# Kernel tuning notes

Measured on AMD Instinct MI355X. Metric: run time of the kernel, lower is better.

## Reference

```python
import jax, jax.numpy as jnp
import numpy as np

B, C, H, W = 16, 256, 32, 32
K = 3          # kernel size
KK = K * K     # matrix_batch = 9 kernel positions
N = 256        # out_channels = n (power of 2, nstack = 1)


def setup_inputs() -> dict:
    key = jax.random.key(0)
    k1, k2, k3, k4 = jax.random.split(key, 4)
    s = 1.0 / np.sqrt(2.0)  # repo's 'regular' param init scale
    return {
        "x": jax.random.normal(k1, (B, C, H, W), jnp.float32),
        "twiddle1": jax.random.normal(k2, (KK, N - 1, 2, 2), jnp.float32) * s,
        "twiddle2": jax.random.normal(k3, (KK, N - 1, 2, 2), jnp.float32) * s,
        "bias": jax.random.normal(k4, (KK, N), jnp.float32) * 0.01,
    }


def _butterfly_tied(twiddle, x, increasing):
    """Tied-weight butterfly multiply.
    twiddle: (s, n-1, 2, 2); x: (b, s, n). At stride st, twiddle[:, st-1:2*st-1]
    (length st) is shared across the n/(2*st) blocks (matches butterfly_mult_torch).
    """
    b, s, n = x.shape
    m = n.bit_length() - 1  # log2(n)
    strides = [1 << i for i in range(m)]
    if not increasing:
        strides = strides[::-1]
    for st in strides:
        t = twiddle[:, st - 1:2 * st - 1]            # (s, st, 2, 2)
        xr = x.reshape(b, s, n // (2 * st), 2, st)   # (b, s, g, 2, st)
        # out[b,s,g,i,l] = sum_k t[s,l,i,k] * xr[b,s,g,k,l]
        x = jnp.einsum('slik,bsgkl->bsgil', t, xr).reshape(b, s, n)
    return x


def reference(x, twiddle1, twiddle2, bias):
    b, c, h, w = x.shape
    # im2col / F.unfold with kernel 3, pad 1, stride 1 -> (b, c, 9, h*w),
    # kernel positions in row-major order (matches torch unfold layout).
    xp = jnp.pad(x, ((0, 0), (0, 0), (1, 1), (1, 1)))
    patches = jnp.stack(
        [xp[:, :, i:i + h, j:j + w] for i in range(K) for j in range(K)], axis=2
    )  # (b, c, 9, h, w)
    inp = patches.reshape(b, c, KK, h * w).transpose(0, 3, 2, 1)
    inp = inp.reshape(b * h * w, KK, c)  # (batch*h*w, 9, c)
    # BB^T: B^T (decreasing stride) then B (increasing stride), bias on last.
    y = _butterfly_tied(twiddle1, inp, increasing=False)
    y = _butterfly_tied(twiddle2, y, increasing=True) + bias  # bias: (9, N)
    out = y.mean(axis=1)  # average over the 9 kernel positions -> (b*h*w, N)
    return out.reshape(b, h * w, N).transpose(0, 2, 1).reshape(b, N, h, w)
```

## Files before the change

kernel.cpp:

```cpp
#include <hip/hip_runtime.h>
#include <hip/hip_bf16.h>

typedef __attribute__((ext_vector_type(8))) short short8;
typedef __attribute__((ext_vector_type(4))) float float4v;

#define XT_ELEMS (16*34*34*256)
#define WG_ELEMS (9*4*2*8*128*8)
#define XT_BYTES (XT_ELEMS*2)
#define WG_BYTES (WG_ELEMS*2)

__global__ __launch_bounds__(256) void k_transpose(const float* __restrict__ x,
                                                   __hip_bfloat16* __restrict__ xT) {
  __shared__ float tile[256 * 33];
  int blk = blockIdx.x;
  int h = blk & 31, b = blk >> 5;
  int tid = threadIdx.x;
  {
    int w4 = (tid & 7) * 4, c0 = tid >> 3;
#pragma unroll
    for (int j = 0; j < 8; ++j) {
      int ci = c0 + 32 * j;
      float4 v = *(const float4*)&x[((b * 256 + ci) * 32 + h) * 32 + w4];
      *(float4*)&tile[ci * 33 + w4] = v;
    }
  }
  __syncthreads();
  {
    int c2 = (tid & 127) * 2, wbase = (tid >> 7) * 16;
#pragma unroll
    for (int i = 0; i < 16; ++i) {
      int w = wbase + i;
      __hip_bfloat162 pk;
      pk.x = __float2bfloat16(tile[c2 * 33 + w]);
      pk.y = __float2bfloat16(tile[(c2 + 1) * 33 + w]);
      *(__hip_bfloat162*)&xT[((b * 34 + h + 1) * 34 + (w + 1)) * 256 + c2] = pk;
    }
  }
  if (h < 2) {
    uint4 z4 = {0u, 0u, 0u, 0u};
    int edge = h * 33;
    uint4* rowp = (uint4*)&xT[((b * 34 + edge) * 34) * 256];
    for (int i = tid; i < 1088; i += 256) rowp[i] = z4;
    for (int i = tid; i < 1024; i += 256) {
      int hh = 1 + (i >> 5);
      int c16 = (i & 31) * 8;
      *(uint4*)&xT[((b * 34 + hh) * 34 + edge) * 256 + c16] = z4;
    }
  }
}

__global__ __launch_bounds__(256) void k_build_w(const float* __restrict__ tw1,
                                                 const float* __restrict__ tw2,
                                                 const float* __restrict__ bias,
                                                 __hip_bfloat16* __restrict__ Wg,
                                                 float* __restrict__ biasout) {
  __shared__ float mat[256 * 17];
  __shared__ __align__(16) float tws[2 * 255 * 4];
  int blk = blockIdx.x;
  int tid = threadIdx.x;
  if (blk == 144) {
    if (tid < 256) {
      float a = 0.f;
#pragma unroll
      for (int s = 0; s < 9; ++s) a += bias[s * 256 + tid];
      biasout[tid] = a * (1.f / 9.f);
    }
    return;
  }
  int sidx = blk >> 4;
  int colbase = (blk & 15) * 16;

  for (int i = tid; i < 255 * 4; i += 256) {
    tws[i]           = tw1[sidx * 255 * 4 + i];
    tws[255 * 4 + i] = tw2[sidx * 255 * 4 + i];
  }
  {
    int r = tid;
#pragma unroll
    for (int c = 0; c < 16; ++c) mat[r * 17 + c] = (r == colbase + c) ? 1.f : 0.f;
  }

  int c  = tid & 15;
  int pg = tid >> 4;
  for (int ph = 0; ph < 2; ++ph) {
    for (int si = 0; si < 8; ++si) {
      int lg = ph ? si : (7 - si);
      int st = 1 << lg;
      __syncthreads();
      float x0[8], x1[8], t0[8], t1[8], t2[8], t3[8];
#pragma unroll
      for (int i = 0; i < 8; ++i) {
        int qp = pg * 8 + i;
        int li = qp & (st - 1);
        int gi = qp >> lg;
        int p0 = (gi << (lg + 1)) | li;
        int p1 = p0 + st;
        float4 tv = *(const float4*)&tws[(ph * 255 + st - 1 + li) * 4];
        t0[i] = tv.x; t1[i] = tv.y; t2[i] = tv.z; t3[i] = tv.w;
        x0[i] = mat[p0 * 17 + c];
        x1[i] = mat[p1 * 17 + c];
      }
#pragma unroll
      for (int i = 0; i < 8; ++i) {
        int qp = pg * 8 + i;
        int li = qp & (st - 1);
        int gi = qp >> lg;
        int p0 = (gi << (lg + 1)) | li;
        int p1 = p0 + st;
        mat[p0 * 17 + c] = t0[i] * x0[i] + t1[i] * x1[i];
        mat[p1 * 17 + c] = t2[i] * x0[i] + t3[i] * x1[i];
      }
    }
  }
  __syncthreads();

  for (int idx = tid; idx < 256 * 16; idx += 256) {
    int r = idx >> 4, cc = idx & 15;
    int cg = colbase + cc;
    int pr = cg >> 6, qq = (cg >> 3) & 7, c8 = cg & 7;
    int nt = r >> 7, nl = r & 127;
    int o = ((((sidx * 4 + pr) * 2 + nt) * 8 + qq) * 128 + nl) * 8 + c8;
    Wg[o] = __float2bfloat16(mat[r * 17 + cc] * (1.f / 9.f));
  }
}

#define LDS_A_SZ 16384
#define LDS_B_SZ (8 * 204 * 16)

__global__ __launch_bounds__(256) void k_gemm(const __hip_bfloat16* __restrict__ xT,
                                              const __hip_bfloat16* __restrict__ Wg,
                                              const float* __restrict__ biasout,
                                              float* __restrict__ out) {
  __shared__ __align__(16) char lds[2 * LDS_A_SZ + LDS_B_SZ];
  const char* WgB = (const char*)Wg;
  const char* xTB = (const char*)xT;

  int blk = blockIdx.x;
  int nt = blk & 1;
  int pt = blk >> 1;
  int b  = pt >> 3;
  int h0 = (pt & 7) * 4;

  int tid  = threadIdx.x;
  int lane = tid & 63;
  int wave = tid >> 6;
  int wm = wave >> 1, wn = wave & 1;
  int q = lane >> 4, l16 = lane & 15;

  float4v acc[4][4];
#pragma unroll
  for (int r = 0; r < 4; ++r)
#pragma unroll
    for (int j = 0; j < 4; ++j) acc[r][j] = (float4v){0.f, 0.f, 0.f, 0.f};

  auto stage_a = [&](int step, int buf) {
    int p = step / 9, s = step - p * 9;
    const char* g = WgB + (((s * 4 + p) * 2 + nt) * 16384);
#pragma unroll
    for (int i = 0; i < 4; ++i) {
      int slotbase = i * 256 + wave * 64;
      __builtin_amdgcn_global_load_lds(
          (const __attribute__((address_space(1))) void*)(g + (slotbase + lane) * 16),
          (__attribute__((address_space(3))) void*)(lds + buf * LDS_A_SZ + slotbase * 16),
          16, 0, 0);
    }
  };

  auto stage_b = [&](int p) {
#pragma unroll
    for (int i = 0; i < 7; ++i) {
      int slot = i * 256 + tid;
      if (slot < 1632) {
        int qq  = slot / 204;
        int pos = slot - qq * 204;
        int hh  = pos / 34;
        int ww  = pos - hh * 34;
        const char* g = xTB + (((b * 34 + h0 + hh) * 34 + ww) * 256 +
                               p * 64 + qq * 8) * 2;
        __builtin_amdgcn_global_load_lds(
            (const __attribute__((address_space(1))) void*)g,
            (__attribute__((address_space(3))) void*)(lds + 2 * LDS_A_SZ +
                                                     (i * 256 + wave * 64) * 16),
            16, 0, 0);
      }
    }
  };

  auto do_step = [&](int step) {
    int p = step / 9, s = step - p * 9;
    int si = s / 3, sj = s - si * 3;
    const char* Ab = lds + (step & 1) * LDS_A_SZ;
    const char* Bb = lds + 2 * LDS_A_SZ;
    short8 af[8], bfr[8];
#pragma unroll
    for (int r = 0; r < 4; ++r) {
      int nl = wm * 64 + r * 16 + l16;
      af[r]     = *(const short8*)(Ab + (q * 128 + nl) * 16);
      af[r + 4] = *(const short8*)(Ab + ((q + 4) * 128 + nl) * 16);
    }
#pragma unroll
    for (int j = 0; j < 4; ++j) {
      int pp = wn * 64 + j * 16 + l16;
      int pos = ((pp >> 5) + si) * 34 + (pp & 31) + sj;
      bfr[j]     = *(const short8*)(Bb + (q * 204 + pos) * 16);
      bfr[j + 4] = *(const short8*)(Bb + ((q + 4) * 204 + pos) * 16);
    }
#pragma unroll
    for (int r = 0; r < 4; ++r)
#pragma unroll
      for (int j = 0; j < 4; ++j) {
        acc[r][j] = __builtin_amdgcn_mfma_f32_16x16x32_bf16(af[r], bfr[j], acc[r][j], 0, 0, 0);
        acc[r][j] = __builtin_amdgcn_mfma_f32_16x16x32_bf16(af[r + 4], bfr[j + 4], acc[r][j], 0, 0, 0);
      }
  };

  stage_a(0, 0);
  stage_b(0);
  __syncthreads();
  for (int step = 0; step < 36; ++step) {
    int p = step / 9, s = step - p * 9;
    if (s == 8) {
      if (p < 3) stage_a(step + 1, (step + 1) & 1);
      do_step(step);
      __syncthreads();
      if (p < 3) { stage_b(p + 1); __syncthreads(); }
    } else {
      stage_a(step + 1, (step + 1) & 1);
      do_step(step);
      __syncthreads();
    }
  }

  int nbase = nt * 128 + wm * 64;
#pragma unroll
  for (int j = 0; j < 4; ++j) {
    int pp = wn * 64 + j * 16 + l16;
    int hr = h0 + (pp >> 5), wc = pp & 31;
#pragma unroll
    for (int r = 0; r < 4; ++r) {
      float4v v = acc[r][j];
#pragma unroll
      for (int reg = 0; reg < 4; ++reg) {
        int n = nbase + r * 16 + q * 4 + reg;
        out[((b * 256 + n) * 32 + hr) * 32 + wc] = v[reg] + biasout[n];
      }
    }
  }
}

extern "C" void kernel_launch(void* const* d_in, const int* in_sizes, int n_in,
                              void* d_out, int out_size, void* d_ws, size_t ws_size,
                              hipStream_t stream) {
  const float* x    = (const float*)d_in[0];
  const float* tw1  = (const float*)d_in[1];
  const float* tw2  = (const float*)d_in[2];
  const float* bias = (const float*)d_in[3];
  float* out = (float*)d_out;

  char* ws = (char*)d_ws;
  __hip_bfloat16* xT = (__hip_bfloat16*)ws;
  __hip_bfloat16* Wg = (__hip_bfloat16*)(ws + XT_BYTES);
  float* biasout     = (float*)(ws + XT_BYTES + WG_BYTES);

  k_transpose<<<512, 256, 0, stream>>>(x, xT);
  k_build_w<<<145, 256, 0, stream>>>(tw1, tw2, bias, Wg, biasout);
  k_gemm<<<256, 256, 0, stream>>>(xT, Wg, biasout, out);
}
```

Baseline: 127.1 us.

## Split K across two wave groups in GEMM with LDS reduction

Doubles the GEMM workgroup to 512 threads (8 waves). The two halves of the K dimension within each 64-channel chunk go to separate wave groups, which then reduce their accumulators through LDS and each write half of the output. LDS fragment offsets are also precomputed outside the step loop. The aim is to double waves per CU for better latency hiding, since there are only 256 blocks. The cost is extra barriers and a reduction epilogue, and register pressure under launch bounds (512,2).

Measured after the change: 264.6 us. 108% more time.

```diff
diff --git a/kernel.cpp b/kernel.cpp
--- a/kernel.cpp
+++ b/kernel.cpp
@@ -127,10 +127,10 @@
 #define LDS_A_SZ 16384
 #define LDS_B_SZ (8 * 204 * 16)
 
-__global__ __launch_bounds__(256) void k_gemm(const __hip_bfloat16* __restrict__ xT,
-                                              const __hip_bfloat16* __restrict__ Wg,
-                                              const float* __restrict__ biasout,
-                                              float* __restrict__ out) {
+__global__ __launch_bounds__(512, 2) void k_gemm(const __hip_bfloat16* __restrict__ xT,
+                                                 const __hip_bfloat16* __restrict__ Wg,
+                                                 const float* __restrict__ biasout,
+                                                 float* __restrict__ out) {
   __shared__ __align__(16) char lds[2 * LDS_A_SZ + LDS_B_SZ];
   const char* WgB = (const char*)Wg;
   const char* xTB = (const char*)xT;
@@ -144,21 +144,35 @@
   int tid  = threadIdx.x;
   int lane = tid & 63;
   int wave = tid >> 6;
-  int wm = wave >> 1, wn = wave & 1;
-  int q = lane >> 4, l16 = lane & 15;
+  int wk = wave >> 2;
+  int wm = (wave >> 1) & 1;
+  int wn = wave & 1;
+  int q0 = lane >> 4;
+  int q  = q0 + wk * 4;
+  int l16 = lane & 15;
 
   float4v acc[4][4];
 #pragma unroll
   for (int r = 0; r < 4; ++r)
 #pragma unroll
     for (int j = 0; j < 4; ++j) acc[r][j] = (float4v){0.f, 0.f, 0.f, 0.f};
+
+  int aoff[4];
+#pragma unroll
+  for (int r = 0; r < 4; ++r) aoff[r] = (q * 128 + wm * 64 + r * 16 + l16) * 16;
+  int boff[4];
+#pragma unroll
+  for (int j = 0; j < 4; ++j) {
+    int p = wn * 64 + j * 16 + l16;
+    boff[j] = 2 * LDS_A_SZ + (q * 204 + (p >> 5) * 34 + (p & 31)) * 16;
+  }
 
   auto stage_a = [&](int step, int buf) {
     int p = step / 9, s = step - p * 9;
     const char* g = WgB + (((s * 4 + p) * 2 + nt) * 16384);
 #pragma unroll
-    for (int i = 0; i < 4; ++i) {
-      int slotbase = i * 256 + wave * 64;
+    for (int i = 0; i < 2; ++i) {
+      int slotbase = i * 512 + wave * 64;
       __builtin_amdgcn_global_load_lds(
           (const __attribute__((address_space(1))) void*)(g + (slotbase + lane) * 16),
           (__attribute__((address_space(3))) void*)(lds + buf * LDS_A_SZ + slotbase * 16),
@@ -168,8 +182,8 @@
 
   auto stage_b = [&](int p) {
 #pragma unroll
-    for (int i = 0; i < 7; ++i) {
-      int slot = i * 256 + tid;
+    for (int i = 0; i < 4; ++i) {
+      int slot = i * 512 + tid;
       if (slot < 1632) {
         int qq  = slot / 204;
         int pos = slot - qq * 204;
@@ -180,7 +194,7 @@
         __builtin_amdgcn_global_load_lds(
             (const __attribute__((address_space(1))) void*)g,
             (__attribute__((address_space(3))) void*)(lds + 2 * LDS_A_SZ +
-                                                     (i * 256 + wave * 64) * 16),
+                                                     (i * 512 + wave * 64) * 16),
             16, 0, 0);
       }
     }
@@ -189,29 +203,18 @@
   auto do_step = [&](int step) {
     int p = step / 9, s = step - p * 9;
     int si = s / 3, sj = s - si * 3;
-    const char* Ab = lds + (step & 1) * LDS_A_SZ;
-    const char* Bb = lds + 2 * LDS_A_SZ;
-    short8 af[8], bfr[8];
-#pragma unroll
-    for (int r = 0; r < 4; ++r) {
-      int nl = wm * 64 + r * 16 + l16;
-      af[r]     = *(const short8*)(Ab + (q * 128 + nl) * 16);
-      af[r + 4] = *(const short8*)(Ab + ((q + 4) * 128 + nl) * 16);
-    }
-#pragma unroll
-    for (int j = 0; j < 4; ++j) {
-      int pp = wn * 64 + j * 16 + l16;
-      int pos = ((pp >> 5) + si) * 34 + (pp & 31) + sj;
-      bfr[j]     = *(const short8*)(Bb + (q * 204 + pos) * 16);
-      bfr[j + 4] = *(const short8*)(Bb + ((q + 4) * 204 + pos) * 16);
-    }
+    int soff = (si * 34 + sj) * 16;
+    int abase = (step & 1) * LDS_A_SZ;
+    short8 af[4], bfr[4];
+#pragma unroll
+    for (int r = 0; r < 4; ++r) af[r] = *(const short8*)(lds + abase + aoff[r]);
+#pragma unroll
+    for (int j = 0; j < 4; ++j) bfr[j] = *(const short8*)(lds + boff[j] + soff);
 #pragma unroll
     for (int r = 0; r < 4; ++r)
 #pragma unroll
-      for (int j = 0; j < 4; ++j) {
+      for (int j = 0; j < 4; ++j)
         acc[r][j] = __builtin_amdgcn_mfma_f32_16x16x32_bf16(af[r], bfr[j], acc[r][j], 0, 0, 0);
-        acc[r][j] = __builtin_amdgcn_mfma_f32_16x16x32_bf16(af[r + 4], bfr[j + 4], acc[r][j], 0, 0, 0);
-      }
   };
 
   stage_a(0, 0);
@@ -231,9 +234,46 @@
     }
   }
 
+  {
+    int pr = wm * 2 + wn;
+    __syncthreads();
+    if (wk == 1) {
+#pragma unroll
+      for (int r = 0; r < 4; ++r)
+#pragma unroll
+        for (int jj = 0; jj < 2; ++jj)
+          *(float4v*)(lds + (((pr * 4 + r) * 2 + jj) * 64 + lane) * 16) = acc[r][jj];
+    }
+    __syncthreads();
+    if (wk == 0) {
+#pragma unroll
+      for (int r = 0; r < 4; ++r)
+#pragma unroll
+        for (int jj = 0; jj < 2; ++jj)
+          acc[r][jj] += *(const float4v*)(lds + (((pr * 4 + r) * 2 + jj) * 64 + lane) * 16);
+    }
+    __syncthreads();
+    if (wk == 0) {
+#pragma unroll
+      for (int r = 0; r < 4; ++r)
+#pragma unroll
+        for (int jj = 0; jj < 2; ++jj)
+          *(float4v*)(lds + (((pr * 4 + r) * 2 + jj) * 64 + lane) * 16) = acc[r][2 + jj];
+    }
+    __syncthreads();
+    if (wk == 1) {
+#pragma unroll
+      for (int r = 0; r < 4; ++r)
+#pragma unroll
+        for (int jj = 0; jj < 2; ++jj)
+          acc[r][2 + jj] += *(const float4v*)(lds + (((pr * 4 + r) * 2 + jj) * 64 + lane) * 16);
+    }
+  }
+
   int nbase = nt * 128 + wm * 64;
 #pragma unroll
-  for (int j = 0; j < 4; ++j) {
+  for (int jj = 0; jj < 2; ++jj) {
+    int j = wk * 2 + jj;
     int pp = wn * 64 + j * 16 + l16;
     int hr = h0 + (pp >> 5), wc = pp & 31;
 #pragma unroll
@@ -241,7 +281,7 @@
       float4v v = acc[r][j];
 #pragma unroll
       for (int reg = 0; reg < 4; ++reg) {
-        int n = nbase + r * 16 + q * 4 + reg;
+        int n = nbase + r * 16 + q0 * 4 + reg;
         out[((b * 256 + n) * 32 + hr) * 32 + wc] = v[reg] + biasout[n];
       }
     }
@@ -264,5 +304,5 @@
 
   k_transpose<<<512, 256, 0, stream>>>(x, xT);
   k_build_w<<<145, 256, 0, stream>>>(tw1, tw2, bias, Wg, biasout);
-  k_gemm<<<256, 256, 0, stream>>>(xT, Wg, biasout, out);
+  k_gemm<<<256, 512, 0, stream>>>(xT, Wg, biasout, out);
 }
```

## Restructure GEMM into split-K waves with 32x32 MFMA and direct B loads

Applied to the files above, without the earlier changes.

The GEMM is retiled to 1024 smaller blocks (64 output channels by 64 pixels). The four waves split the K dimension by channel group and are combined through an LDS reduction at the end. The activation layout changes to channel-group-major, so each lane loads its B fragments straight from global memory into registers, replacing the shared B tile staging. This moves from 16x16x32 to 32x32x16 MFMA with a smaller A buffer, aiming for more occupancy and fewer LDS round trips. The cost is extra reduction synchronisation and uncoalesced, possibly redundant global B reads.

Result: faster. 119.0 us (-6.4%).

```diff
diff --git a/kernel.cpp b/kernel.cpp
--- a/kernel.cpp
+++ b/kernel.cpp
@@ -2,16 +2,15 @@
 #include <hip/hip_bf16.h>
 
 typedef __attribute__((ext_vector_type(8))) short short8;
-typedef __attribute__((ext_vector_type(4))) float float4v;
-
-#define XT_ELEMS (16*34*34*256)
-#define WG_ELEMS (9*4*2*8*128*8)
-#define XT_BYTES (XT_ELEMS*2)
-#define WG_BYTES (WG_ELEMS*2)
+typedef __attribute__((ext_vector_type(16))) float float16v;
+
+#define XT_BYTES (16*32*34*34*8*2)
+#define WG_BYTES (9*4*4*8*64*8*2)
 
 __global__ __launch_bounds__(256) void k_transpose(const float* __restrict__ x,
-                                                   __hip_bfloat16* __restrict__ xT) {
+                                                   __hip_bfloat16* __restrict__ xTg) {
   __shared__ float tile[256 * 33];
+  char* xTB = (char*)xTg;
   int blk = blockIdx.x;
   int h = blk & 31, b = blk >> 5;
   int tid = threadIdx.x;
@@ -26,25 +25,27 @@
   }
   __syncthreads();
   {
-    int c2 = (tid & 127) * 2, wbase = (tid >> 7) * 16;
-#pragma unroll
-    for (int i = 0; i < 16; ++i) {
-      int w = wbase + i;
-      __hip_bfloat162 pk;
-      pk.x = __float2bfloat16(tile[c2 * 33 + w]);
-      pk.y = __float2bfloat16(tile[(c2 + 1) * 33 + w]);
-      *(__hip_bfloat162*)&xT[((b * 34 + h + 1) * 34 + (w + 1)) * 256 + c2] = pk;
+    int g0 = tid >> 5, w = tid & 31;
+#pragma unroll
+    for (int gi = 0; gi < 4; ++gi) {
+      int g = gi * 8 + g0;
+      union { short8 s; __hip_bfloat16 hv[8]; } pk;
+#pragma unroll
+      for (int cc = 0; cc < 8; ++cc)
+        pk.hv[cc] = __float2bfloat16(tile[(g * 8 + cc) * 33 + w]);
+      *(short8*)(xTB + ((((b * 32 + g) * 34 + h + 1) * 34) + (w + 1)) * 16) = pk.s;
     }
   }
   if (h < 2) {
     uint4 z4 = {0u, 0u, 0u, 0u};
     int edge = h * 33;
-    uint4* rowp = (uint4*)&xT[((b * 34 + edge) * 34) * 256];
-    for (int i = tid; i < 1088; i += 256) rowp[i] = z4;
-    for (int i = tid; i < 1024; i += 256) {
-      int hh = 1 + (i >> 5);
-      int c16 = (i & 31) * 8;
-      *(uint4*)&xT[((b * 34 + hh) * 34 + edge) * 256 + c16] = z4;
+    for (int i = tid; i < 32 * 34; i += 256) {
+      int g = i / 34, w = i - g * 34;
+      *(uint4*)(xTB + ((((b * 32 + g) * 34 + edge) * 34) + w) * 16) = z4;
+    }
+    for (int i = tid; i < 32 * 32; i += 256) {
+      int g = i >> 5, hh = 1 + (i & 31);
+      *(uint4*)(xTB + ((((b * 32 + g) * 34 + hh) * 34) + edge) * 16) = z4;
     }
   }
 }
@@ -117,132 +118,117 @@
   for (int idx = tid; idx < 256 * 16; idx += 256) {
     int r = idx >> 4, cc = idx & 15;
     int cg = colbase + cc;
-    int pr = cg >> 6, qq = (cg >> 3) & 7, c8 = cg & 7;
-    int nt = r >> 7, nl = r & 127;
-    int o = ((((sidx * 4 + pr) * 2 + nt) * 8 + qq) * 128 + nl) * 8 + c8;
+    int pr = cg >> 6, g = (cg >> 3) & 7, c8 = cg & 7;
+    int nq = r >> 6, nl = r & 63;
+    int o = ((((sidx * 4 + pr) * 4 + nq) * 8 + g) * 64 + nl) * 8 + c8;
     Wg[o] = __float2bfloat16(mat[r * 17 + cc] * (1.f / 9.f));
   }
 }
 
-#define LDS_A_SZ 16384
-#define LDS_B_SZ (8 * 204 * 16)
-
-__global__ __launch_bounds__(256) void k_gemm(const __hip_bfloat16* __restrict__ xT,
-                                              const __hip_bfloat16* __restrict__ Wg,
-                                              const float* __restrict__ biasout,
-                                              float* __restrict__ out) {
-  __shared__ __align__(16) char lds[2 * LDS_A_SZ + LDS_B_SZ];
+#define ABUF 8192
+
+__global__ __launch_bounds__(256, 4) void k_gemm(const __hip_bfloat16* __restrict__ xTg,
+                                                 const __hip_bfloat16* __restrict__ Wg,
+                                                 const float* __restrict__ biasout,
+                                                 float* __restrict__ out) {
+  __shared__ __align__(64) char lds[2 * ABUF];
   const char* WgB = (const char*)Wg;
-  const char* xTB = (const char*)xT;
+  const char* xTB = (const char*)xTg;
 
   int blk = blockIdx.x;
-  int nt = blk & 1;
-  int pt = blk >> 1;
-  int b  = pt >> 3;
-  int h0 = (pt & 7) * 4;
+  int nq = blk & 3;
+  int pt = (blk >> 2) & 15;
+  int b  = blk >> 6;
+  int h0 = pt * 2;
 
   int tid  = threadIdx.x;
   int lane = tid & 63;
-  int wave = tid >> 6;
-  int wm = wave >> 1, wn = wave & 1;
-  int q = lane >> 4, l16 = lane & 15;
-
-  float4v acc[4][4];
-#pragma unroll
-  for (int r = 0; r < 4; ++r)
-#pragma unroll
-    for (int j = 0; j < 4; ++j) acc[r][j] = (float4v){0.f, 0.f, 0.f, 0.f};
+  int wk   = tid >> 6;
+  int half = lane >> 5;
+  int l31  = lane & 31;
+
+  float16v acc[2][2];
+#pragma unroll
+  for (int mt = 0; mt < 2; ++mt)
+#pragma unroll
+    for (int p2 = 0; p2 < 2; ++p2)
+#pragma unroll
+      for (int e = 0; e < 16; ++e) acc[mt][p2][e] = 0.f;
+
+  int aoff[2];
+#pragma unroll
+  for (int mt = 0; mt < 2; ++mt)
+    aoff[mt] = ((2 * wk + half) * 64 + mt * 32 + l31) * 16;
+
+  int bbase = ((b * 32 + 2 * wk + half) * 34 + h0) * 34 + l31;
 
   auto stage_a = [&](int step, int buf) {
     int p = step / 9, s = step - p * 9;
-    const char* g = WgB + (((s * 4 + p) * 2 + nt) * 16384);
-#pragma unroll
-    for (int i = 0; i < 4; ++i) {
-      int slotbase = i * 256 + wave * 64;
+    const char* g = WgB + ((s * 4 + p) * 4 + nq) * 8192;
+#pragma unroll
+    for (int i = 0; i < 2; ++i) {
+      int slotbase = i * 256 + wk * 64;
       __builtin_amdgcn_global_load_lds(
           (const __attribute__((address_space(1))) void*)(g + (slotbase + lane) * 16),
-          (__attribute__((address_space(3))) void*)(lds + buf * LDS_A_SZ + slotbase * 16),
+          (__attribute__((address_space(3))) void*)(lds + buf * ABUF + slotbase * 16),
           16, 0, 0);
     }
   };
 
-  auto stage_b = [&](int p) {
-#pragma unroll
-    for (int i = 0; i < 7; ++i) {
-      int slot = i * 256 + tid;
-      if (slot < 1632) {
-        int qq  = slot / 204;
-        int pos = slot - qq * 204;
-        int hh  = pos / 34;
-        int ww  = pos - hh * 34;
-        const char* g = xTB + (((b * 34 + h0 + hh) * 34 + ww) * 256 +
-                               p * 64 + qq * 8) * 2;
-        __builtin_amdgcn_global_load_lds(
-            (const __attribute__((address_space(1))) void*)g,
-            (__attribute__((address_space(3))) void*)(lds + 2 * LDS_A_SZ +
-                                                     (i * 256 + wave * 64) * 16),
-            16, 0, 0);
-      }
-    }
-  };
-
-  auto do_step = [&](int step) {
+  auto load_b = [&](int step, short8* bf) {
     int p = step / 9, s = step - p * 9;
     int si = s / 3, sj = s - si * 3;
-    const char* Ab = lds + (step & 1) * LDS_A_SZ;
-    const char* Bb = lds + 2 * LDS_A_SZ;
-    short8 af[8], bfr[8];
-#pragma unroll
-    for (int r = 0; r < 4; ++r) {
-      int nl = wm * 64 + r * 16 + l16;
-      af[r]     = *(const short8*)(Ab + (q * 128 + nl) * 16);
-      af[r + 4] = *(const short8*)(Ab + ((q + 4) * 128 + nl) * 16);
-    }
-#pragma unroll
-    for (int j = 0; j < 4; ++j) {
-      int pp = wn * 64 + j * 16 + l16;
-      int pos = ((pp >> 5) + si) * 34 + (pp & 31) + sj;
-      bfr[j]     = *(const short8*)(Bb + (q * 204 + pos) * 16);
-      bfr[j + 4] = *(const short8*)(Bb + ((q + 4) * 204 + pos) * 16);
-    }
-#pragma unroll
-    for (int r = 0; r < 4; ++r)
-#pragma unroll
-      for (int j = 0; j < 4; ++j) {
-        acc[r][j] = __builtin_amdgcn_mfma_f32_16x16x32_bf16(af[r], bfr[j], acc[r][j], 0, 0, 0);
-        acc[r][j] = __builtin_amdgcn_mfma_f32_16x16x32_bf16(af[r + 4], bfr[j + 4], acc[r][j], 0, 0, 0);
-      }
+    int off = (bbase + p * (8 * 34 * 34) + si * 34 + sj) * 16;
+    bf[0] = *(const short8*)(xTB + off);
+    bf[1] = *(const short8*)(xTB + off + 34 * 16);
   };
 
+  short8 bcur[2], bnext[2];
   stage_a(0, 0);
-  stage_b(0);
-  __syncthreads();
+  load_b(0, bcur);
+  __syncthreads();
+
   for (int step = 0; step < 36; ++step) {
-    int p = step / 9, s = step - p * 9;
-    if (s == 8) {
-      if (p < 3) stage_a(step + 1, (step + 1) & 1);
-      do_step(step);
-      __syncthreads();
-      if (p < 3) { stage_b(p + 1); __syncthreads(); }
-    } else {
+    if (step < 35) {
       stage_a(step + 1, (step + 1) & 1);
-      do_step(step);
-      __syncthreads();
-    }
-  }
-
-  int nbase = nt * 128 + wm * 64;
-#pragma unroll
-  for (int j = 0; j < 4; ++j) {
-    int pp = wn * 64 + j * 16 + l16;
-    int hr = h0 + (pp >> 5), wc = pp & 31;
-#pragma unroll
-    for (int r = 0; r < 4; ++r) {
-      float4v v = acc[r][j];
-#pragma unroll
-      for (int reg = 0; reg < 4; ++reg) {
-        int n = nbase + r * 16 + q * 4 + reg;
-        out[((b * 256 + n) * 32 + hr) * 32 + wc] = v[reg] + biasout[n];
+      load_b(step + 1, bnext);
+    }
+    int abase = (step & 1) * ABUF;
+    short8 af0 = *(const short8*)(lds + abase + aoff[0]);
+    short8 af1 = *(const short8*)(lds + abase + aoff[1]);
+    acc[0][0] = __builtin_amdgcn_mfma_f32_32x32x16_bf16(af0, bcur[0], acc[0][0], 0, 0, 0);
+    acc[0][1] = __builtin_amdgcn_mfma_f32_32x32x16_bf16(af0, bcur[1], acc[0][1], 0, 0, 0);
+    acc[1][0] = __builtin_amdgcn_mfma_f32_32x32x16_bf16(af1, bcur[0], acc[1][0], 0, 0, 0);
+    acc[1][1] = __builtin_amdgcn_mfma_f32_32x32x16_bf16(af1, bcur[1], acc[1][1], 0, 0, 0);
+    __syncthreads();
+    bcur[0] = bnext[0];
+    bcur[1] = bnext[1];
+  }
+
+  auto fptr = [&](int slot) { return (float16v*)(lds + slot * 4096 + lane * 64); };
+  __syncthreads();
+  if (wk >= 2) { *fptr((wk - 2) * 2 + 0) = acc[0][0]; *fptr((wk - 2) * 2 + 1) = acc[0][1]; }
+  __syncthreads();
+  if (wk < 2)  { acc[0][0] += *fptr(wk * 2 + 0); acc[0][1] += *fptr(wk * 2 + 1); }
+  __syncthreads();
+  if (wk >= 2) { *fptr((wk - 2) * 2 + 0) = acc[1][0]; *fptr((wk - 2) * 2 + 1) = acc[1][1]; }
+  __syncthreads();
+  if (wk < 2)  { acc[1][0] += *fptr(wk * 2 + 0); acc[1][1] += *fptr(wk * 2 + 1); }
+  __syncthreads();
+  if (wk == 1) { *fptr(0) = acc[0][0]; *fptr(1) = acc[0][1];
+                 *fptr(2) = acc[1][0]; *fptr(3) = acc[1][1]; }
+  __syncthreads();
+  if (wk == 0) {
+    acc[0][0] += *fptr(0); acc[0][1] += *fptr(1);
+    acc[1][0] += *fptr(2); acc[1][1] += *fptr(3);
+#pragma unroll
+    for (int mt = 0; mt < 2; ++mt) {
+#pragma unroll
+      for (int reg = 0; reg < 16; ++reg) {
+        int n = nq * 64 + mt * 32 + (reg & 3) + 8 * (reg >> 2) + 4 * half;
+        float bv = biasout[n];
+        out[((b * 256 + n) * 32 + h0) * 32 + l31]     = acc[mt][0][reg] + bv;
+        out[((b * 256 + n) * 32 + h0 + 1) * 32 + l31] = acc[mt][1][reg] + bv;
       }
     }
   }
@@ -258,11 +244,11 @@
   float* out = (float*)d_out;
 
   char* ws = (char*)d_ws;
-  __hip_bfloat16* xT = (__hip_bfloat16*)ws;
-  __hip_bfloat16* Wg = (__hip_bfloat16*)(ws + XT_BYTES);
-  float* biasout     = (float*)(ws + XT_BYTES + WG_BYTES);
-
-  k_transpose<<<512, 256, 0, stream>>>(x, xT);
+  __hip_bfloat16* xTg = (__hip_bfloat16*)ws;
+  __hip_bfloat16* Wg  = (__hip_bfloat16*)(ws + XT_BYTES);
+  float* biasout      = (float*)(ws + XT_BYTES + WG_BYTES);
+
+  k_transpose<<<512, 256, 0, stream>>>(x, xTg);
   k_build_w<<<145, 256, 0, stream>>>(tw1, tw2, bias, Wg, biasout);
-  k_gemm<<<256, 256, 0, stream>>>(xT, Wg, biasout, out);
-}
+  k_gemm<<<1024, 256, 0, stream>>>(xTg, Wg, biasout, out);
+}
```
